# Performance work log

Measured on AMD Instinct MI355X. Metric: run time of the kernel, lower is better.

Reference implementation:

```python
import jax, jax.numpy as jnp
import numpy as np
from jax import lax

NW_LIST = [4, 8, 12]   # num_windows_list for num_windows=8
HEADS = 4
EPS = 1e-5             # BatchNorm eps (eval mode, running_mean=0, running_var=1)


def conv2d(x, w, pad):
    return lax.conv_general_dilated(x, w, (1, 1), [(pad, pad), (pad, pad)],
                                    dimension_numbers=('NCHW', 'OIHW', 'NCHW'))


def bn(x, g, b):
    # eval-mode BatchNorm with running_mean=0, running_var=1
    s = g / np.sqrt(1.0 + EPS)
    return x * s[None, :, None, None] + b[None, :, None, None]


def psa(x, q_w, k_w, v_w, proj_w):
    # multi-head spatial self-attention within a window, residual output
    B, C, h, w = x.shape
    L = h * w
    hd = C // HEADS
    q = conv2d(x, q_w, 0).reshape(B, HEADS, hd, L)
    k = conv2d(x, k_w, 0).reshape(B, HEADS, hd, L)
    v = conv2d(x, v_w, 0).reshape(B, HEADS, hd, L)
    attn = jax.nn.softmax(jnp.einsum('bhdl,bhdm->bhlm', q, k) * (hd ** -0.5), axis=-1)
    o = jnp.einsum('bhlm,bhdm->bhdl', attn, v).reshape(B, C, h, w)
    return conv2d(o, proj_w, 0) + x


def dpconv_forward(x, conv1_w, bn1_g, bn1_b, conv2_w, bn2_g, bn2_b,
                   conv3_w, bn3_g, bn3_b, pos_w, bnp_g, bnp_b,
                   q_w, k_w, v_w, proj_w):
    x1 = bn(conv2d(x, conv1_w, 0), bn1_g, bn1_b)
    chunks = jnp.split(x1, 3, axis=1)
    N, Cb, H, W = chunks[0].shape
    outs = []
    for nw, xc in zip(NW_LIST, chunks):
        sh, sw = H // nw, W // nw
        kh, kw = sh + H % nw, sw + W % nw
        hh = (np.arange(nw) * sh)[:, None] + np.arange(kh)   # [nw, kh] static indices
        ww = (np.arange(nw) * sw)[:, None] + np.arange(kw)   # [nw, kw]
        # unfold: [N,Cb,nw,kh,nw,kw] -> torch layout [N, Cb*kh*kw, L]
        p = xc[:, :, hh[:, :, None, None], ww[None, None, :, :]]
        u = p.transpose(0, 1, 3, 5, 2, 4).reshape(N, Cb * kh * kw, nw * nw)
        uw = u.reshape(-1, Cb, kh, kw)   # mirrors torch .view(-1, C, kh, kw)
        att = psa(uw, q_w, k_w, v_w, proj_w) + bn(conv2d(uw, pos_w, 1), bnp_g, bnp_b)
        y = att.reshape(N, Cb, kh, kw, nw, nw).transpose(0, 1, 4, 2, 5, 3)
        folded = jnp.zeros((N, Cb, H, W), x.dtype).at[
            :, :, hh[:, :, None, None], ww[None, None, :, :]].add(y)
        cnt = jnp.zeros((H, W), x.dtype).at[
            hh[:, :, None, None], ww[None, None, :, :]].add(
            jnp.ones((nw, kh, nw, kw), x.dtype))
        outs.append(folded / cnt[None, None])
    cat = jnp.concatenate(outs, axis=1)
    h2 = bn(conv2d(cat, conv2_w, 1), bn2_g, bn2_b) + x1
    return bn(conv2d(h2, conv3_w, 1), bn3_g, bn3_b)


def setup_inputs() -> dict:
    key = jax.random.key(0)
    ks = jax.random.split(key, 10)
    C, Cb = 192, 64
    inp = {
        'x': jax.random.normal(ks[0], (2, C, 100, 100), jnp.float32),
        'conv1_w': jax.random.normal(ks[1], (C, C, 1, 1), jnp.float32) * 0.05,
        'bn1_g': jnp.ones((C,), jnp.float32), 'bn1_b': jnp.zeros((C,), jnp.float32),
        'conv2_w': jax.random.normal(ks[2], (C, C, 3, 3), jnp.float32) * 0.05,
        'bn2_g': jnp.ones((C,), jnp.float32), 'bn2_b': jnp.zeros((C,), jnp.float32),
        'conv3_w': jax.random.normal(ks[3], (C, C, 3, 3), jnp.float32) * 0.05,
        'bn3_g': jnp.ones((C,), jnp.float32), 'bn3_b': jnp.zeros((C,), jnp.float32),
        'pos_w': jax.random.normal(ks[4], (Cb, Cb, 3, 3), jnp.float32) * 0.05,
        'bnp_g': jnp.ones((Cb,), jnp.float32), 'bnp_b': jnp.zeros((Cb,), jnp.float32),
        'q_w': jax.random.normal(ks[5], (Cb, Cb, 1, 1), jnp.float32) * 0.05,
        'k_w': jax.random.normal(ks[6], (Cb, Cb, 1, 1), jnp.float32) * 0.05,
        'v_w': jax.random.normal(ks[7], (Cb, Cb, 1, 1), jnp.float32) * 0.05,
        'proj_w': jax.random.normal(ks[8], (Cb, Cb, 1, 1), jnp.float32) * 0.05,
    }
    return inp


def reference(x, conv1_w, bn1_g, bn1_b, conv2_w, bn2_g, bn2_b,
              conv3_w, bn3_g, bn3_b, pos_w, bnp_g, bnp_b,
              q_w, k_w, v_w, proj_w):
    return dpconv_forward(x, conv1_w, bn1_g, bn1_b, conv2_w, bn2_g, bn2_b,
                          conv3_w, bn3_g, bn3_b, pos_w, bnp_g, bnp_b,
                          q_w, k_w, v_w, proj_w)
```

## Files before the change

### kernel.cpp

```cpp
#include <hip/hip_runtime.h>
#include <hip/hip_bf16.h>

#define N_ 2
#define C_ 192
#define CB_ 64
#define HW_ 100
#define PIX_ (HW_*HW_)
#define PADW_ 102
#define PADPIX_ (PADW_*PADW_)
#define KTOT_ 1728
#define KPOS_ 576
#define QSCALE_ 0.3606737602222409f

typedef __attribute__((ext_vector_type(8))) short bf16x8;
typedef __attribute__((ext_vector_type(4))) short bf16x4;
typedef __attribute__((ext_vector_type(4))) float f32x4;

#if defined(__has_builtin)
#if __has_builtin(__builtin_amdgcn_mfma_f32_16x16x16bf16_1k)
#define HAVE_MFMA16 1
#endif
#if __has_builtin(__builtin_amdgcn_exp2f)
#define EXP2(x) __builtin_amdgcn_exp2f(x)
#endif
#endif
#ifndef EXP2
#define EXP2(x) exp2f(x)
#endif

static __device__ __forceinline__ float bn_scale(float g) {
    return g * rsqrtf(1.0f + 1e-5f);
}

static __device__ __forceinline__ unsigned short f2bf(float v) {
    __hip_bfloat16 h = __float2bfloat16(v);
    return *(unsigned short*)&h;
}

__global__ __launch_bounds__(256) void x_nhwc_k(
    const float* __restrict__ in, unsigned short* __restrict__ out)
{
    int idx = blockIdx.x * 256 + threadIdx.x;
    if (idx >= N_ * 4 * PIX_) return;
    int p     = idx % PIX_;
    int chunk = (idx / PIX_) & 3;
    int n     = idx / (PIX_ * 4);
    int c0 = chunk * 48;
    const float* ip = in + ((size_t)n * C_ + c0) * PIX_ + p;
    unsigned short vals[48];
    #pragma unroll
    for (int j = 0; j < 48; ++j) vals[j] = f2bf(ip[(size_t)j * PIX_]);
    unsigned short* op = out + ((size_t)n * PIX_ + p) * 192 + c0;
    #pragma unroll
    for (int v = 0; v < 6; ++v) {
        bf16x8 pack;
        #pragma unroll
        for (int j = 0; j < 8; ++j) pack[j] = (short)vals[v * 8 + j];
        *(bf16x8*)(op + v * 8) = pack;
    }
}

__global__ __launch_bounds__(256) void conv1x1_mfma_k(
    const unsigned short* __restrict__ Xc,
    const float* __restrict__ w,
    const float* __restrict__ g, const float* __restrict__ bb,
    float* __restrict__ out)
{
    __shared__ unsigned short lds[64][72];
    int tid  = threadIdx.x;
    int lane = tid & 63;
    int wv   = tid >> 6;
    int c    = lane & 15;
    int g8   = (lane >> 4) * 8;
    int p0   = blockIdx.x * 64;
    int co0  = blockIdx.y * 64;
    int n    = blockIdx.z;

    int sp = tid >> 2;
    int sk = (tid & 3) * 8;
    int pc = min(p0 + sp, PIX_ - 1);
    const unsigned short* bp = Xc + ((size_t)n * PIX_ + pc) * 192;

    const float* arow = w + (size_t)(co0 + wv * 16 + c) * C_;

    f32x4 acc[4];
    #pragma unroll
    for (int f = 0; f < 4; ++f) acc[f] = (f32x4){0.f, 0.f, 0.f, 0.f};

    bf16x8 b0 = *(const bf16x8*)(bp + sk);
    bf16x8 b1 = *(const bf16x8*)(bp + 32 + sk);

    for (int k0 = 0; k0 < C_; k0 += 64) {
        __syncthreads();
        *(bf16x8*)(&lds[sp][sk])      = b0;
        *(bf16x8*)(&lds[sp][32 + sk]) = b1;
        __syncthreads();
        if (k0 + 64 < C_) {
            b0 = *(const bf16x8*)(bp + k0 + 64 + sk);
            b1 = *(const bf16x8*)(bp + k0 + 96 + sk);
        }
        #pragma unroll
        for (int h = 0; h < 2; ++h) {
            bf16x8 a;
            const float* ap = arow + k0 + h * 32 + g8;
            #pragma unroll
            for (int j = 0; j < 8; ++j) a[j] = (short)f2bf(ap[j]);
            #pragma unroll
            for (int f = 0; f < 4; ++f) {
                bf16x8 b = *(const bf16x8*)(&lds[f * 16 + c][h * 32 + g8]);
                acc[f] = __builtin_amdgcn_mfma_f32_16x16x32_bf16(a, b, acc[f], 0, 0, 0);
            }
        }
    }

    #pragma unroll
    for (int f = 0; f < 4; ++f) {
        int p = p0 + f * 16 + c;
        if (p < PIX_) {
            #pragma unroll
            for (int r = 0; r < 4; ++r) {
                int co = co0 + wv * 16 + (lane >> 4) * 4 + r;
                out[(size_t)(n * C_ + co) * PIX_ + p] = acc[f][r] * bn_scale(g[co]) + bb[co];
            }
        }
    }
}

__global__ __launch_bounds__(256) void wcvt_all_k(
    const float* __restrict__ pw, const float* __restrict__ w2,
    const float* __restrict__ w3,
    unsigned short* __restrict__ pwb, unsigned short* __restrict__ w2b,
    unsigned short* __restrict__ w3b)
{
    int idx = blockIdx.x * 256 + threadIdx.x;
    const int S0 = CB_ * KPOS_;
    const int S1 = S0 + C_ * KTOT_;
    const int S2 = S1 + C_ * KTOT_;
    if (idx < S0) {
        int t = idx % 9, ci = (idx / 9) % CB_, co = idx / (9 * CB_);
        pwb[(size_t)co * KPOS_ + t * CB_ + ci] = f2bf(pw[idx]);
    } else if (idx < S1) {
        int k = idx - S0;
        int t = k % 9, ci = (k / 9) % C_, co = k / (9 * C_);
        w2b[(size_t)co * KTOT_ + t * C_ + ci] = f2bf(w2[k]);
    } else if (idx < S2) {
        int k = idx - S1;
        int t = k % 9, ci = (k / 9) % C_, co = k / (9 * C_);
        w3b[(size_t)co * KTOT_ + t * C_ + ci] = f2bf(w3[k]);
    }
}

template<int NW, int SH, int KH>
__device__ __forceinline__ void gather_body(
    const float* __restrict__ x1, float* __restrict__ U, int f, int cidx)
{
    int t = f;
    int j = t % NW; t /= NW;
    int i = t % NW; t /= NW;
    int c = t % KH; t /= KH;
    int r = t % KH; t /= KH;
    int cb = t % CB_;
    int n  = t / CB_;
    int hh = i * SH + r;
    int ww = j * SH + c;
    U[f] = x1[((n * C_ + cidx * CB_ + cb) * HW_ + hh) * HW_ + ww];
}

__global__ __launch_bounds__(256) void gather_c_k(
    const float* __restrict__ x1, float* __restrict__ Uall)
{
    int gid = blockIdx.x * 256 + threadIdx.x;
    if (gid < 1280000)       gather_body<4, 25, 25>(x1, Uall,            gid,            0);
    else if (gid < 3377152)  gather_body<8, 12, 16>(x1, Uall + 1280000,  gid - 1280000,  1);
    else if (gid < 6031360)  gather_body<12, 8, 12>(x1, Uall + 3377152,  gid - 3377152,  2);
}

template<int L, int LP, int NPIX>
__device__ __forceinline__ void qkv_body(
    unsigned short (*lds)[72],
    const float* __restrict__ U,
    const float* __restrict__ qw, const float* __restrict__ kw,
    const float* __restrict__ vw,
    unsigned short* __restrict__ Q, unsigned short* __restrict__ Kt,
    unsigned short* __restrict__ V, int bid)
{
    int tid  = threadIdx.x;
    int lane = tid & 63;
    int wv   = tid >> 6;
    int c    = lane & 15;
    int g8   = (lane >> 4) * 8;
    int q0   = bid * 64;

    int sp = tid >> 2;
    int sk = (tid & 3) * 8;
    int qc = min(q0 + sp, NPIX - 1);
    int b  = qc / L, p = qc % L;
    const float* ub = U + (size_t)b * 64 * L + p;

    bf16x8 b0, b1;
    #pragma unroll
    for (int j = 0; j < 8; ++j) {
        b0[j] = (short)f2bf(ub[(size_t)(sk + j) * L]);
        b1[j] = (short)f2bf(ub[(size_t)(32 + sk + j) * L]);
    }
    __syncthreads();
    *(bf16x8*)(&lds[sp][sk])      = b0;
    *(bf16x8*)(&lds[sp][32 + sk]) = b1;
    __syncthreads();

    f32x4 acc[3][4];
    #pragma unroll
    for (int s = 0; s < 3; ++s)
        #pragma unroll
        for (int f = 0; f < 4; ++f) acc[s][f] = (f32x4){0.f, 0.f, 0.f, 0.f};

    const float* wbase[3] = {qw, kw, vw};
    #pragma unroll
    for (int s = 0; s < 3; ++s) {
        const float* arow = wbase[s] + (size_t)(wv * 16 + c) * 64;
        #pragma unroll
        for (int h = 0; h < 2; ++h) {
            bf16x8 a;
            const float* ap = arow + h * 32 + g8;
            #pragma unroll
            for (int j = 0; j < 8; ++j) a[j] = (short)f2bf(ap[j]);
            #pragma unroll
            for (int f = 0; f < 4; ++f) {
                bf16x8 bfr = *(const bf16x8*)(&lds[f * 16 + c][h * 32 + g8]);
                acc[s][f] = __builtin_amdgcn_mfma_f32_16x16x32_bf16(a, bfr, acc[s][f], 0, 0, 0);
            }
        }
    }

    #pragma unroll
    for (int f = 0; f < 4; ++f) {
        int qq = q0 + f * 16 + c;
        if (qq < NPIX) {
            int bo = qq / L, po = qq % L;
            #pragma unroll
            for (int r = 0; r < 4; ++r) {
                int co = wv * 16 + (lane >> 4) * 4 + r;
                Q[(size_t)(bo * 64 + co) * L + po] = f2bf(acc[0][f][r] * QSCALE_);
                Kt[((size_t)(bo * 4 + wv) * L + po) * 16 + ((lane >> 4) * 4 + r)] = f2bf(acc[1][f][r]);
                V[(size_t)(bo * 64 + co) * LP + po] = f2bf(acc[2][f][r]);
            }
        }
    }
}

__global__ __launch_bounds__(256) void qkv_c_k(
    const float* __restrict__ Uall,
    const float* __restrict__ qw, const float* __restrict__ kw,
    const float* __restrict__ vw,
    unsigned short* __restrict__ Qa, unsigned short* __restrict__ Ka,
    unsigned short* __restrict__ Va)
{
    __shared__ unsigned short lds[64][72];
    int bid = blockIdx.x;
    if (bid < 313)
        qkv_body<625, 632, 20000>(lds, Uall, qw, kw, vw, Qa, Ka, Va, bid);
    else if (bid < 825)
        qkv_body<256, 256, 32768>(lds, Uall + 1280000, qw, kw, vw,
                                  Qa + 1280000, Ka + 1280000, Va + 1294336, bid - 313);
    else
        qkv_body<144, 144, 41472>(lds, Uall + 3377152, qw, kw, vw,
                                  Qa + 3377152, Ka + 3377152, Va + 3391488, bid - 825);
}

template<int L, int LP, int NMT>
__device__ __forceinline__ void attn_body(
    const unsigned short* __restrict__ Q, const unsigned short* __restrict__ Kt,
    const unsigned short* __restrict__ V, unsigned short* __restrict__ O,
    int lblk, int bh)
{
    int tid  = threadIdx.x;
    int lane = tid & 63;
    int wv   = tid >> 6;
    int c    = lane & 15;
    int g    = lane >> 4;
    int b = bh >> 2, h = bh & 3;
    const unsigned short* qb = Q + (size_t)(b * 64 + h * 16) * L;
    const unsigned short* kb = Kt + (size_t)bh * L * 16;
    const unsigned short* vb = V + (size_t)(b * 64 + h * 16) * LP + (size_t)c * LP;
    unsigned short* ob = O + (size_t)(b * 64 + h * 16) * L;

    int l = lblk * 64 + wv * 16 + c;
    bool lval = (l < L);
    int lc = lval ? l : (L - 1);

    f32x4 acc = (f32x4){0.f, 0.f, 0.f, 0.f};
    float mrun = -1e30f, srun = 0.f;

#ifdef HAVE_MFMA16
    bf16x4 qf;
    #pragma unroll
    for (int j = 0; j < 4; ++j) qf[j] = (short)qb[(g * 4 + j) * L + lc];
#else
    bf16x8 qf = (bf16x8){0,0,0,0,0,0,0,0};
    if (g < 2) {
        #pragma unroll
        for (int j = 0; j < 8; ++j) qf[j] = (short)qb[(g * 8 + j) * L + lc];
    }
#endif

    for (int mt = 0; mt < NMT; ++mt) {
        int m0 = mt * 64;
        bool full = (m0 + 64 <= L);

        f32x4 s[4];
#ifdef HAVE_MFMA16
        #pragma unroll
        for (int t = 0; t < 4; ++t) {
            int mm = full ? (m0 + c + t * 16) : min(m0 + c + t * 16, L - 1);
            bf16x4 kf = *(const bf16x4*)(kb + (size_t)mm * 16 + g * 4);
            s[t] = __builtin_amdgcn_mfma_f32_16x16x16bf16_1k(
                kf, qf, (f32x4){0.f,0.f,0.f,0.f}, 0, 0, 0);
        }
#else
        #pragma unroll
        for (int t = 0; t < 4; ++t) {
            bf16x8 kf = (bf16x8){0,0,0,0,0,0,0,0};
            if (g < 2) {
                int mm = full ? (m0 + c + t * 16) : min(m0 + c + t * 16, L - 1);
                kf = *(const bf16x8*)(kb + (size_t)mm * 16 + g * 8);
            }
            s[t] = __builtin_amdgcn_mfma_f32_16x16x32_bf16(
                kf, qf, (f32x4){0.f,0.f,0.f,0.f}, 0, 0, 0);
        }
#endif

        float p[16];
        float tmax = -1e30f;
        #pragma unroll
        for (int t = 0; t < 4; ++t) {
            #pragma unroll
            for (int r = 0; r < 4; ++r) {
                int m = m0 + t * 16 + g * 4 + r;
                float v = s[t][r];
                if (!full && m >= L) v = -1e30f;
                p[t * 4 + r] = v;
                tmax = fmaxf(tmax, v);
            }
        }
        tmax = fmaxf(tmax, __shfl_xor(tmax, 16, 64));
        tmax = fmaxf(tmax, __shfl_xor(tmax, 32, 64));
        if (!__all(tmax <= mrun)) {
            float mnew = fmaxf(mrun, tmax);
            float corr = EXP2(mrun - mnew);
            srun *= corr;
            #pragma unroll
            for (int r = 0; r < 4; ++r) acc[r] *= corr;
            mrun = mnew;
        }
        float ps0 = 0.f, ps1 = 0.f, ps2 = 0.f, ps3 = 0.f;
        #pragma unroll
        for (int t = 0; t < 4; ++t) {
            p[t * 4 + 0] = EXP2(p[t * 4 + 0] - mrun); ps0 += p[t * 4 + 0];
            p[t * 4 + 1] = EXP2(p[t * 4 + 1] - mrun); ps1 += p[t * 4 + 1];
            p[t * 4 + 2] = EXP2(p[t * 4 + 2] - mrun); ps2 += p[t * 4 + 2];
            p[t * 4 + 3] = EXP2(p[t * 4 + 3] - mrun); ps3 += p[t * 4 + 3];
        }
        srun += (ps0 + ps1) + (ps2 + ps3);

#ifdef HAVE_MFMA16
        #pragma unroll
        for (int t = 0; t < 4; ++t) {
            bf16x4 pb;
            #pragma unroll
            for (int j = 0; j < 4; ++j) pb[j] = (short)f2bf(p[t * 4 + j]);
            bf16x4 vf = *(const bf16x4*)(vb + m0 + t * 16 + g * 4);
            acc = __builtin_amdgcn_mfma_f32_16x16x16bf16_1k(vf, pb, acc, 0, 0, 0);
        }
#else
        int hi = g >> 1;
        #pragma unroll
        for (int H = 0; H < 2; ++H) {
            bf16x8 pb;
            #pragma unroll
            for (int j = 0; j < 8; ++j) {
                int srcLane = (((2 * g + (j >> 2)) & 3) << 4) | c;
                float v1 = __shfl(p[(H * 2) * 4 + (j & 3)], srcLane, 64);
                float v2 = __shfl(p[(H * 2 + 1) * 4 + (j & 3)], srcLane, 64);
                pb[j] = (short)f2bf(hi ? v2 : v1);
            }
            bf16x8 vf = *(const bf16x8*)(vb + m0 + H * 32 + g * 8);
            acc = __builtin_amdgcn_mfma_f32_16x16x32_bf16(vf, pb, acc, 0, 0, 0);
        }
#endif
    }

    float stot = srun;
    stot += __shfl_xor(stot, 16, 64);
    stot += __shfl_xor(stot, 32, 64);
    float inv = 1.f / stot;
    if (lval) {
        #pragma unroll
        for (int r = 0; r < 4; ++r)
            ob[(size_t)(g * 4 + r) * L + l] = f2bf(acc[r] * inv);
    }
}

__global__ __launch_bounds__(256) void attn_c_k(
    const unsigned short* __restrict__ Qa, const unsigned short* __restrict__ Ka,
    const unsigned short* __restrict__ Va, unsigned short* __restrict__ Oa)
{
    int bid = blockIdx.x;
    if (bid < 1280) {
        attn_body<625, 632, 10>(Qa, Ka, Va, Oa, bid % 10, bid / 10);
    } else if (bid < 3328) {
        int k = bid - 1280;
        attn_body<256, 256, 4>(Qa + 1280000, Ka + 1280000, Va + 1294336,
                               Oa + 1280000, k % 4, k / 4);
    } else {
        int k = bid - 3328;
        attn_body<144, 144, 3>(Qa + 3377152, Ka + 3377152, Va + 3391488,
                               Oa + 3377152, k % 3, k / 3);
    }
}

template<int L, int NPIX>
__device__ __forceinline__ void proj_body(
    unsigned short (*lds)[72],
    const unsigned short* __restrict__ O, const float* __restrict__ U,
    const float* __restrict__ pw, float* __restrict__ A, int bid)
{
    int tid  = threadIdx.x;
    int lane = tid & 63;
    int wv   = tid >> 6;
    int c    = lane & 15;
    int g8   = (lane >> 4) * 8;
    int q0   = bid * 64;

    int sp = tid >> 2;
    int sk = (tid & 3) * 8;
    int qc = min(q0 + sp, NPIX - 1);
    int b  = qc / L, p = qc % L;
    const unsigned short* ob = O + (size_t)b * 64 * L + p;

    bf16x8 b0, b1;
    #pragma unroll
    for (int j = 0; j < 8; ++j) {
        b0[j] = (short)ob[(size_t)(sk + j) * L];
        b1[j] = (short)ob[(size_t)(32 + sk + j) * L];
    }
    __syncthreads();
    *(bf16x8*)(&lds[sp][sk])      = b0;
    *(bf16x8*)(&lds[sp][32 + sk]) = b1;
    __syncthreads();

    f32x4 acc[4];
    #pragma unroll
    for (int f = 0; f < 4; ++f) acc[f] = (f32x4){0.f, 0.f, 0.f, 0.f};

    const float* arow = pw + (size_t)(wv * 16 + c) * 64;
    #pragma unroll
    for (int h = 0; h < 2; ++h) {
        bf16x8 a;
        const float* ap = arow + h * 32 + g8;
        #pragma unroll
        for (int j = 0; j < 8; ++j) a[j] = (short)f2bf(ap[j]);
        #pragma unroll
        for (int f = 0; f < 4; ++f) {
            bf16x8 bfr = *(const bf16x8*)(&lds[f * 16 + c][h * 32 + g8]);
            acc[f] = __builtin_amdgcn_mfma_f32_16x16x32_bf16(a, bfr, acc[f], 0, 0, 0);
        }
    }

    #pragma unroll
    for (int f = 0; f < 4; ++f) {
        int qq = q0 + f * 16 + c;
        if (qq < NPIX) {
            int bo = qq / L, po = qq % L;
            #pragma unroll
            for (int r = 0; r < 4; ++r) {
                int co = wv * 16 + (lane >> 4) * 4 + r;
                size_t oi = (size_t)(bo * 64 + co) * L + po;
                A[oi] = acc[f][r] + U[oi];
            }
        }
    }
}

__global__ __launch_bounds__(256) void proj_c_k(
    const unsigned short* __restrict__ Oa, const float* __restrict__ Uall,
    const float* __restrict__ pw, float* __restrict__ Aa)
{
    __shared__ unsigned short lds[64][72];
    int bid = blockIdx.x;
    if (bid < 313)
        proj_body<625, 20000>(lds, Oa, Uall, pw, Aa, bid);
    else if (bid < 825)
        proj_body<256, 32768>(lds, Oa + 1280000, Uall + 1280000, pw, Aa + 1280000, bid - 313);
    else
        proj_body<144, 41472>(lds, Oa + 3377152, Uall + 3377152, pw, Aa + 3377152, bid - 825);
}

template<int KH, int PW, int L>
__device__ __forceinline__ void padU_body(
    const float* __restrict__ U, unsigned short* __restrict__ Up, int idx)
{
    int pp = idx % (PW * PW);
    int b  = idx / (PW * PW);
    int xx = pp % PW, yy = pp / PW;
    bool inter = (xx >= 1 && xx <= KH && yy >= 1 && yy <= KH);
    const float* up = U + (size_t)b * 64 * L + (yy - 1) * KH + (xx - 1);
    unsigned short vals[64];
    #pragma unroll
    for (int j = 0; j < 64; ++j) vals[j] = inter ? f2bf(up[(size_t)j * L]) : 0;
    unsigned short* op = Up + (size_t)idx * 64;
    #pragma unroll
    for (int v = 0; v < 8; ++v) {
        bf16x8 pack;
        #pragma unroll
        for (int j = 0; j < 8; ++j) pack[j] = (short)vals[v * 8 + j];
        *(bf16x8*)(op + v * 8) = pack;
    }
}

__global__ __launch_bounds__(256) void padU_c_k(
    const float* __restrict__ Uall, unsigned short* __restrict__ Upa)
{
    int idx = blockIdx.x * 256 + threadIdx.x;
    if (idx < 23328)        padU_body<25, 27, 625>(Uall,            Upa,            idx);
    else if (idx < 64800)   padU_body<16, 18, 256>(Uall + 1280000,  Upa + 1492992,  idx - 23328);
    else if (idx < 121248)  padU_body<12, 14, 144>(Uall + 3377152,  Upa + 4147200,  idx - 64800);
}

template<int L, int PW, int KH, int NPIX>
__device__ __forceinline__ void posconv_body(
    unsigned short (*lds)[64][72],
    const unsigned short* __restrict__ Up, const unsigned short* __restrict__ Wb,
    const float* __restrict__ g, const float* __restrict__ bb,
    float* __restrict__ A, int bid)
{
    int tid  = threadIdx.x;
    int lane = tid & 63;
    int wv   = tid >> 6;
    int c    = lane & 15;
    int g8   = (lane >> 4) * 8;
    int p0   = bid * 64;

    int sp = tid >> 2;
    int sk = (tid & 3) * 8;
    int qq0 = p0 + sp;
    int po = 0;
    if (qq0 < NPIX) {
        int b = qq0 / L, p = qq0 % L;
        po = b * PW * PW + (p / KH) * PW + (p % KH);
    }

    const unsigned short* arow = Wb + (size_t)(wv * 16 + c) * KPOS_;

    f32x4 acc[4];
    #pragma unroll
    for (int f = 0; f < 4; ++f) acc[f] = (f32x4){0.f, 0.f, 0.f, 0.f};

    const int NT = KPOS_ / 64;

    bf16x8 b0, b1, a0, a1;
    {
        const unsigned short* bp = Up + ((size_t)po << 6);
        b0 = *(const bf16x8*)(bp + sk);
        b1 = *(const bf16x8*)(bp + 32 + sk);
        *(bf16x8*)(&lds[0][sp][sk])      = b0;
        *(bf16x8*)(&lds[0][sp][32 + sk]) = b1;
    }
    {
        const unsigned short* bp = Up + ((size_t)(po + 1) << 6);
        b0 = *(const bf16x8*)(bp + sk);
        b1 = *(const bf16x8*)(bp + 32 + sk);
    }
    a0 = *(const bf16x8*)(arow + g8);
    a1 = *(const bf16x8*)(arow + 32 + g8);

    for (int t = 0; t < NT; ++t) {
        __syncthreads();
        bf16x8 bf0[4], bf1[4];
        #pragma unroll
        for (int f = 0; f < 4; ++f) {
            bf0[f] = *(const bf16x8*)(&lds[t & 1][f * 16 + c][g8]);
            bf1[f] = *(const bf16x8*)(&lds[t & 1][f * 16 + c][32 + g8]);
        }
        if (t + 1 < NT) {
            *(bf16x8*)(&lds[(t + 1) & 1][sp][sk])      = b0;
            *(bf16x8*)(&lds[(t + 1) & 1][sp][32 + sk]) = b1;
            if (t + 2 < NT) {
                int tap = t + 2;
                int toff = (tap / 3) * PW + (tap % 3);
                const unsigned short* bp = Up + ((size_t)(po + toff) << 6);
                b0 = *(const bf16x8*)(bp + sk);
                b1 = *(const bf16x8*)(bp + 32 + sk);
            }
        }
        bf16x8 a0n, a1n;
        if (t + 1 < NT) {
            a0n = *(const bf16x8*)(arow + (t + 1) * 64 + g8);
            a1n = *(const bf16x8*)(arow + (t + 1) * 64 + 32 + g8);
        }
        #pragma unroll
        for (int f = 0; f < 4; ++f) {
            acc[f] = __builtin_amdgcn_mfma_f32_16x16x32_bf16(a0, bf0[f], acc[f], 0, 0, 0);
            acc[f] = __builtin_amdgcn_mfma_f32_16x16x32_bf16(a1, bf1[f], acc[f], 0, 0, 0);
        }
        a0 = a0n; a1 = a1n;
    }

    #pragma unroll
    for (int f = 0; f < 4; ++f) {
        int q = p0 + f * 16 + c;
        if (q < NPIX) {
            int b = q / L, p = q % L;
            #pragma unroll
            for (int r = 0; r < 4; ++r) {
                int co = wv * 16 + (lane >> 4) * 4 + r;
                A[(size_t)(b * 64 + co) * L + p] += acc[f][r] * bn_scale(g[co]) + bb[co];
            }
        }
    }
}

__global__ __launch_bounds__(256) void posconv_c_k(
    const unsigned short* __restrict__ Upa, const unsigned short* __restrict__ Wb,
    const float* __restrict__ g, const float* __restrict__ bb,
    float* __restrict__ Aa)
{
    __shared__ unsigned short lds[2][64][72];
    int bid = blockIdx.x;
    if (bid < 313)
        posconv_body<625, 27, 25, 20000>(lds, Upa, Wb, g, bb, Aa, bid);
    else if (bid < 825)
        posconv_body<256, 18, 16, 32768>(lds, Upa + 1492992, Wb, g, bb, Aa + 1280000, bid - 313);
    else
        posconv_body<144, 14, 12, 41472>(lds, Upa + 4147200, Wb, g, bb, Aa + 3377152, bid - 825);
}

template<int NW, int SH, int KH>
__device__ __forceinline__ void fold_body(
    const float* __restrict__ A, float* __restrict__ cat, int idx, int cidx)
{
    int w  = idx % HW_;
    int h  = (idx / HW_) % HW_;
    int cb = (idx / PIX_) % CB_;
    int n  = idx / (PIX_ * CB_);
    int numh = h - KH + 1;
    int ilo = numh > 0 ? (numh + SH - 1) / SH : 0;
    int ihi = min(NW - 1, h / SH);
    int numw = w - KH + 1;
    int jlo = numw > 0 ? (numw + SH - 1) / SH : 0;
    int jhi = min(NW - 1, w / SH);
    float sum = 0.f;
    for (int i = ilo; i <= ihi; ++i) {
        int r = h - i * SH;
        for (int j = jlo; j <= jhi; ++j) {
            int c = w - j * SH;
            int f = ((((n * CB_ + cb) * KH + r) * KH + c) * NW + i) * NW + j;
            sum += A[f];
        }
    }
    float cnt = (float)((ihi - ilo + 1) * (jhi - jlo + 1));
    cat[((n * C_ + cidx * CB_ + cb) * HW_ + h) * HW_ + w] = sum / cnt;
}

__global__ __launch_bounds__(256) void fold_c_k(
    const float* __restrict__ Aa, float* __restrict__ cat)
{
    int idx = blockIdx.x * 256 + threadIdx.x;
    if (idx < 1280000)       fold_body<4, 25, 25>(Aa,            cat, idx,            0);
    else if (idx < 2560000)  fold_body<8, 12, 16>(Aa + 1280000,  cat, idx - 1280000,  1);
    else if (idx < 3840000)  fold_body<12, 8, 12>(Aa + 3377152,  cat, idx - 2560000,  2);
}

__global__ __launch_bounds__(256) void pad_nhwc_k(
    const float* __restrict__ in, unsigned short* __restrict__ out)
{
    int idx = blockIdx.x * 256 + threadIdx.x;
    if (idx >= N_ * 4 * PADPIX_) return;
    int pp    = idx % PADPIX_;
    int chunk = (idx / PADPIX_) & 3;
    int n     = idx / (PADPIX_ * 4);
    int xx = pp % PADW_, yy = pp / PADW_;
    int c0 = chunk * 48;
    bool inter = (xx >= 1 && xx <= HW_ && yy >= 1 && yy <= HW_);
    const float* ip = in + ((size_t)n * C_ + c0) * PIX_ + (yy - 1) * HW_ + (xx - 1);
    unsigned short vals[48];
    #pragma unroll
    for (int j = 0; j < 48; ++j) vals[j] = inter ? f2bf(ip[(size_t)j * PIX_]) : 0;
    unsigned short* op = out + ((size_t)n * PADPIX_ + pp) * 192 + c0;
    #pragma unroll
    for (int v = 0; v < 6; ++v) {
        bf16x8 pack;
        #pragma unroll
        for (int j = 0; j < 8; ++j) pack[j] = (short)vals[v * 8 + j];
        *(bf16x8*)(op + v * 8) = pack;
    }
}

__global__ __launch_bounds__(256) void ring_zero_k(unsigned short* __restrict__ Xb)
{
    int idx = blockIdx.x * 256 + threadIdx.x;
    if (idx >= N_ * 404 * 192) return;
    int cc = idx % 192;
    int rp = (idx / 192) % 404;
    int n  = idx / (192 * 404);
    int yy, xx;
    if (rp < 102)      { yy = 0;            xx = rp; }
    else if (rp < 204) { yy = 101;          xx = rp - 102; }
    else if (rp < 304) { yy = rp - 204 + 1; xx = 0; }
    else               { yy = rp - 304 + 1; xx = 101; }
    Xb[((size_t)n * PADPIX_ + yy * PADW_ + xx) * 192 + cc] = 0;
}

#define NB3_ (157*3*2)
template<bool RES, bool TOXB>
__global__ __launch_bounds__(256) void conv3x3_mfma_k(
    const unsigned short* __restrict__ Xp,
    const unsigned short* __restrict__ Wb,
    const float* __restrict__ g, const float* __restrict__ bb,
    const float* __restrict__ res, float* __restrict__ out,
    unsigned short* __restrict__ xout)
{
    __shared__ unsigned short lds[2][64][72];
    int tid  = threadIdx.x;
    int lane = tid & 63;
    int wv   = tid >> 6;
    int c    = lane & 15;
    int g8   = (lane >> 4) * 8;

    const int q = NB3_ / 8, r = NB3_ % 8;
    int gid  = blockIdx.x;
    int xcd  = gid % 8, slot = gid / 8;
    int wgid = (xcd < r) ? xcd * (q + 1) + slot
                         : r * (q + 1) + (xcd - r) * q + slot;
    int co0  = (wgid % 3) * 64;
    int rest = wgid / 3;
    int p0   = (rest % 157) * 64;
    int n    = rest / 157;

    const unsigned short* Xn = Xp + (size_t)n * PADPIX_ * 192;

    int sp = tid >> 2;
    int sk = (tid & 3) * 8;
    int pix = p0 + sp;
    int po = (pix < PIX_) ? (pix / HW_) * PADW_ + (pix % HW_) : 0;

    const unsigned short* arow = Wb + (size_t)(co0 + wv * 16 + c) * KTOT_;

    f32x4 acc[4];
    #pragma unroll
    for (int f = 0; f < 4; ++f) acc[f] = (f32x4){0.f, 0.f, 0.f, 0.f};

    const int NT = KTOT_ / 64;

    bf16x8 b0, b1, a0, a1;
    {
        const unsigned short* bp = Xn + (size_t)po * 192;
        b0 = *(const bf16x8*)(bp + sk);
        b1 = *(const bf16x8*)(bp + 32 + sk);
        *(bf16x8*)(&lds[0][sp][sk])      = b0;
        *(bf16x8*)(&lds[0][sp][32 + sk]) = b1;
    }
    {
        const unsigned short* bp = Xn + (size_t)po * 192 + 64;
        b0 = *(const bf16x8*)(bp + sk);
        b1 = *(const bf16x8*)(bp + 32 + sk);
    }
    a0 = *(const bf16x8*)(arow + g8);
    a1 = *(const bf16x8*)(arow + 32 + g8);

    for (int t = 0; t < NT; ++t) {
        __syncthreads();
        bf16x8 bf0[4], bf1[4];
        #pragma unroll
        for (int f = 0; f < 4; ++f) {
            bf0[f] = *(const bf16x8*)(&lds[t & 1][f * 16 + c][g8]);
            bf1[f] = *(const bf16x8*)(&lds[t & 1][f * 16 + c][32 + g8]);
        }
        if (t + 1 < NT) {
            *(bf16x8*)(&lds[(t + 1) & 1][sp][sk])      = b0;
            *(bf16x8*)(&lds[(t + 1) & 1][sp][32 + sk]) = b1;
            if (t + 2 < NT) {
                int k2 = (t + 2) * 64;
                int tap = k2 / 192;
                int ci0 = k2 - tap * 192;
                int toff = (tap / 3) * PADW_ + (tap % 3);
                const unsigned short* bp = Xn + (size_t)(po + toff) * 192 + ci0;
                b0 = *(const bf16x8*)(bp + sk);
                b1 = *(const bf16x8*)(bp + 32 + sk);
            }
        }
        bf16x8 a0n, a1n;
        if (t + 1 < NT) {
            a0n = *(const bf16x8*)(arow + (t + 1) * 64 + g8);
            a1n = *(const bf16x8*)(arow + (t + 1) * 64 + 32 + g8);
        }
        #pragma unroll
        for (int f = 0; f < 4; ++f) {
            acc[f] = __builtin_amdgcn_mfma_f32_16x16x32_bf16(a0, bf0[f], acc[f], 0, 0, 0);
            acc[f] = __builtin_amdgcn_mfma_f32_16x16x32_bf16(a1, bf1[f], acc[f], 0, 0, 0);
        }
        a0 = a0n; a1 = a1n;
    }

    #pragma unroll
    for (int f = 0; f < 4; ++f) {
        int p = p0 + f * 16 + c;
        if (p < PIX_) {
            if (TOXB) {
                int py = p / HW_, px = p % HW_;
                unsigned short* o = xout +
                    ((size_t)n * PADPIX_ + (py + 1) * PADW_ + (px + 1)) * 192 +
                    co0 + wv * 16 + (lane >> 4) * 4;
                ushort4 pk;
                #pragma unroll
                for (int r2 = 0; r2 < 4; ++r2) {
                    int co = co0 + wv * 16 + (lane >> 4) * 4 + r2;
                    float v = acc[f][r2] * bn_scale(g[co]) + bb[co];
                    if (RES) v += res[(size_t)(n * C_ + co) * PIX_ + p];
                    ((unsigned short*)&pk)[r2] = f2bf(v);
                }
                *(ushort4*)o = pk;
            } else {
                #pragma unroll
                for (int r2 = 0; r2 < 4; ++r2) {
                    int co = co0 + wv * 16 + (lane >> 4) * 4 + r2;
                    float v = acc[f][r2] * bn_scale(g[co]) + bb[co];
                    if (RES) v += res[(size_t)(n * C_ + co) * PIX_ + p];
                    out[(size_t)(n * C_ + co) * PIX_ + p] = v;
                }
            }
        }
    }
}

extern "C" void kernel_launch(void* const* d_in, const int* in_sizes, int n_in,
                              void* d_out, int out_size, void* d_ws, size_t ws_size,
                              hipStream_t stream) {
    const float* x       = (const float*)d_in[0];
    const float* conv1_w = (const float*)d_in[1];
    const float* bn1_g   = (const float*)d_in[2];
    const float* bn1_b   = (const float*)d_in[3];
    const float* conv2_w = (const float*)d_in[4];
    const float* bn2_g   = (const float*)d_in[5];
    const float* bn2_b   = (const float*)d_in[6];
    const float* conv3_w = (const float*)d_in[7];
    const float* bn3_g   = (const float*)d_in[8];
    const float* bn3_b   = (const float*)d_in[9];
    const float* pos_w   = (const float*)d_in[10];
    const float* bnp_g   = (const float*)d_in[11];
    const float* bnp_b   = (const float*)d_in[12];
    const float* q_w     = (const float*)d_in[13];
    const float* k_w     = (const float*)d_in[14];
    const float* v_w     = (const float*)d_in[15];
    const float* proj_w  = (const float*)d_in[16];

    float* ws = (float*)d_ws;
    float* x1   = ws;
    float* cat  = ws + 3840000;
    unsigned short* Xc    = (unsigned short*)(ws + 7680000);
    float* Uall = ws + 9600000;
    unsigned short* Oall  = (unsigned short*)(ws + 15640000);
    float* Aall = ws + 21680000;
    unsigned short* Qall  = (unsigned short*)(ws + 27720000);
    unsigned short* Ktall = (unsigned short*)(ws + 30740000);
    unsigned short* Vall  = (unsigned short*)(ws + 33760000);
    unsigned short* Upall = (unsigned short*)(ws + 36790000);
    unsigned short* pwb   = (unsigned short*)(ws + 40670000);
    unsigned short* w2b   = (unsigned short*)(ws + 40690000);
    unsigned short* w3b   = (unsigned short*)(ws + 40856000);
    unsigned short* Xb    = (unsigned short*)(ws + 41022000);
    unsigned short* Xb2   = (unsigned short*)(ws + 43020000);

    x_nhwc_k<<<(N_ * 4 * PIX_ + 255) / 256, 256, 0, stream>>>(x, Xc);
    conv1x1_mfma_k<<<dim3(157, 3, 2), 256, 0, stream>>>(Xc, conv1_w, bn1_g, bn1_b, x1);
    wcvt_all_k<<<(700416 + 255) / 256, 256, 0, stream>>>(pos_w, conv2_w, conv3_w, pwb, w2b, w3b);

    gather_c_k<<<(6031360 + 255) / 256, 256, 0, stream>>>(x1, Uall);
    qkv_c_k<<<1473, 256, 0, stream>>>(Uall, q_w, k_w, v_w, Qall, Ktall, Vall);
    attn_c_k<<<6784, 256, 0, stream>>>(Qall, Ktall, Vall, Oall);
    proj_c_k<<<1473, 256, 0, stream>>>(Oall, Uall, proj_w, Aall);
    padU_c_k<<<(121248 + 255) / 256, 256, 0, stream>>>(Uall, Upall);
    posconv_c_k<<<1473, 256, 0, stream>>>(Upall, pwb, bnp_g, bnp_b, Aall);
    fold_c_k<<<(3840000 + 255) / 256, 256, 0, stream>>>(Aall, cat);

    pad_nhwc_k<<<(N_ * 4 * PADPIX_ + 255) / 256, 256, 0, stream>>>(cat, Xb);
    ring_zero_k<<<(N_ * 404 * 192 + 255) / 256, 256, 0, stream>>>(Xb2);
    conv3x3_mfma_k<true, true><<<NB3_, 256, 0, stream>>>(
        Xb, w2b, bn2_g, bn2_b, x1, nullptr, Xb2);
    conv3x3_mfma_k<false, false><<<NB3_, 256, 0, stream>>>(
        Xb2, w3b, bn3_g, bn3_b, nullptr, (float*)d_out, nullptr);
}
```

Before: 305.2 us.

## Process two query tiles per wave in attention to reuse K/V loads

Each wave in the windowed attention kernel now handles two 16-query chunks, 64 rows apart, so every block covers 128 query positions instead of 64. Each K and V fragment loaded from global memory feeds two MFMA chains, and the online-softmax state is kept per chunk. The grid shrinks to match the new coverage. The cost is higher register pressure, and more wasted work in the smallest window group, where 144 queries are padded to 256.

```diff
diff --git a/kernel.cpp b/kernel.cpp
--- a/kernel.cpp
+++ b/kernel.cpp
@@ -284,22 +284,39 @@
     const unsigned short* vb = V + (size_t)(b * 64 + h * 16) * LP + (size_t)c * LP;
     unsigned short* ob = O + (size_t)(b * 64 + h * 16) * L;
 
-    int l = lblk * 64 + wv * 16 + c;
-    bool lval = (l < L);
-    int lc = lval ? l : (L - 1);
-
-    f32x4 acc = (f32x4){0.f, 0.f, 0.f, 0.f};
-    float mrun = -1e30f, srun = 0.f;
+    int lbase = lblk * 128 + wv * 16 + c;
+    int l[2] = {lbase, lbase + 64};
+    bool lval[2];
+    int lc[2];
+    #pragma unroll
+    for (int ch = 0; ch < 2; ++ch) {
+        lval[ch] = (l[ch] < L);
+        lc[ch] = lval[ch] ? l[ch] : (L - 1);
+    }
+
+    f32x4 acc[2];
+    float mrun[2], srun[2];
+    #pragma unroll
+    for (int ch = 0; ch < 2; ++ch) {
+        acc[ch] = (f32x4){0.f, 0.f, 0.f, 0.f};
+        mrun[ch] = -1e30f; srun[ch] = 0.f;
+    }
 
 #ifdef HAVE_MFMA16
-    bf16x4 qf;
-    #pragma unroll
-    for (int j = 0; j < 4; ++j) qf[j] = (short)qb[(g * 4 + j) * L + lc];
+    bf16x4 qf[2];
+    #pragma unroll
+    for (int ch = 0; ch < 2; ++ch)
+        #pragma unroll
+        for (int j = 0; j < 4; ++j) qf[ch][j] = (short)qb[(g * 4 + j) * L + lc[ch]];
 #else
-    bf16x8 qf = (bf16x8){0,0,0,0,0,0,0,0};
-    if (g < 2) {
-        #pragma unroll
-        for (int j = 0; j < 8; ++j) qf[j] = (short)qb[(g * 8 + j) * L + lc];
+    bf16x8 qf[2];
+    #pragma unroll
+    for (int ch = 0; ch < 2; ++ch) {
+        qf[ch] = (bf16x8){0,0,0,0,0,0,0,0};
+        if (g < 2) {
+            #pragma unroll
+            for (int j = 0; j < 8; ++j) qf[ch][j] = (short)qb[(g * 8 + j) * L + lc[ch]];
+        }
     }
 #endif
 
@@ -307,14 +324,21 @@
         int m0 = mt * 64;
         bool full = (m0 + 64 <= L);
 
-        f32x4 s[4];
+        float p[2][16];
 #ifdef HAVE_MFMA16
         #pragma unroll
         for (int t = 0; t < 4; ++t) {
             int mm = full ? (m0 + c + t * 16) : min(m0 + c + t * 16, L - 1);
             bf16x4 kf = *(const bf16x4*)(kb + (size_t)mm * 16 + g * 4);
-            s[t] = __builtin_amdgcn_mfma_f32_16x16x16bf16_1k(
-                kf, qf, (f32x4){0.f,0.f,0.f,0.f}, 0, 0, 0);
+            f32x4 s0 = __builtin_amdgcn_mfma_f32_16x16x16bf16_1k(
+                kf, qf[0], (f32x4){0.f,0.f,0.f,0.f}, 0, 0, 0);
+            f32x4 s1 = __builtin_amdgcn_mfma_f32_16x16x16bf16_1k(
+                kf, qf[1], (f32x4){0.f,0.f,0.f,0.f}, 0, 0, 0);
+            #pragma unroll
+            for (int r = 0; r < 4; ++r) {
+                p[0][t * 4 + r] = s0[r];
+                p[1][t * 4 + r] = s1[r];
+            }
         }
 #else
         #pragma unroll
@@ -324,79 +348,98 @@
                 int mm = full ? (m0 + c + t * 16) : min(m0 + c + t * 16, L - 1);
                 kf = *(const bf16x8*)(kb + (size_t)mm * 16 + g * 8);
             }
-            s[t] = __builtin_amdgcn_mfma_f32_16x16x32_bf16(
-                kf, qf, (f32x4){0.f,0.f,0.f,0.f}, 0, 0, 0);
+            f32x4 s0 = __builtin_amdgcn_mfma_f32_16x16x32_bf16(
+                kf, qf[0], (f32x4){0.f,0.f,0.f,0.f}, 0, 0, 0);
+            f32x4 s1 = __builtin_amdgcn_mfma_f32_16x16x32_bf16(
+                kf, qf[1], (f32x4){0.f,0.f,0.f,0.f}, 0, 0, 0);
+            #pragma unroll
+            for (int r = 0; r < 4; ++r) {
+                p[0][t * 4 + r] = s0[r];
+                p[1][t * 4 + r] = s1[r];
+            }
         }
 #endif
 
-        float p[16];
-        float tmax = -1e30f;
+        #pragma unroll
+        for (int ch = 0; ch < 2; ++ch) {
+            float tmax = -1e30f;
+            #pragma unroll
+            for (int t = 0; t < 4; ++t) {
+                #pragma unroll
+                for (int r = 0; r < 4; ++r) {
+                    int m = m0 + t * 16 + g * 4 + r;
+                    float v = p[ch][t * 4 + r];
+                    if (!full && m >= L) v = -1e30f;
+                    p[ch][t * 4 + r] = v;
+                    tmax = fmaxf(tmax, v);
+                }
+            }
+            tmax = fmaxf(tmax, __shfl_xor(tmax, 16, 64));
+            tmax = fmaxf(tmax, __shfl_xor(tmax, 32, 64));
+            if (!__all(tmax <= mrun[ch])) {
+                float mnew = fmaxf(mrun[ch], tmax);
+                float corr = EXP2(mrun[ch] - mnew);
+                srun[ch] *= corr;
+                #pragma unroll
+                for (int r = 0; r < 4; ++r) acc[ch][r] *= corr;
+                mrun[ch] = mnew;
+            }
+            float ps0 = 0.f, ps1 = 0.f, ps2 = 0.f, ps3 = 0.f;
+            #pragma unroll
+            for (int t = 0; t < 4; ++t) {
+                p[ch][t * 4 + 0] = EXP2(p[ch][t * 4 + 0] - mrun[ch]); ps0 += p[ch][t * 4 + 0];
+                p[ch][t * 4 + 1] = EXP2(p[ch][t * 4 + 1] - mrun[ch]); ps1 += p[ch][t * 4 + 1];
+                p[ch][t * 4 + 2] = EXP2(p[ch][t * 4 + 2] - mrun[ch]); ps2 += p[ch][t * 4 + 2];
+                p[ch][t * 4 + 3] = EXP2(p[ch][t * 4 + 3] - mrun[ch]); ps3 += p[ch][t * 4 + 3];
+            }
+            srun[ch] += (ps0 + ps1) + (ps2 + ps3);
+        }
+
+#ifdef HAVE_MFMA16
         #pragma unroll
         for (int t = 0; t < 4; ++t) {
-            #pragma unroll
-            for (int r = 0; r < 4; ++r) {
-                int m = m0 + t * 16 + g * 4 + r;
-                float v = s[t][r];
-                if (!full && m >= L) v = -1e30f;
-                p[t * 4 + r] = v;
-                tmax = fmaxf(tmax, v);
-            }
-        }
-        tmax = fmaxf(tmax, __shfl_xor(tmax, 16, 64));
-        tmax = fmaxf(tmax, __shfl_xor(tmax, 32, 64));
-        if (!__all(tmax <= mrun)) {
-            float mnew = fmaxf(mrun, tmax);
-            float corr = EXP2(mrun - mnew);
-            srun *= corr;
-            #pragma unroll
-            for (int r = 0; r < 4; ++r) acc[r] *= corr;
-            mrun = mnew;
-        }
-        float ps0 = 0.f, ps1 = 0.f, ps2 = 0.f, ps3 = 0.f;
-        #pragma unroll
-        for (int t = 0; t < 4; ++t) {
-            p[t * 4 + 0] = EXP2(p[t * 4 + 0] - mrun); ps0 += p[t * 4 + 0];
-            p[t * 4 + 1] = EXP2(p[t * 4 + 1] - mrun); ps1 += p[t * 4 + 1];
-            p[t * 4 + 2] = EXP2(p[t * 4 + 2] - mrun); ps2 += p[t * 4 + 2];
-            p[t * 4 + 3] = EXP2(p[t * 4 + 3] - mrun); ps3 += p[t * 4 + 3];
-        }
-        srun += (ps0 + ps1) + (ps2 + ps3);
-
-#ifdef HAVE_MFMA16
-        #pragma unroll
-        for (int t = 0; t < 4; ++t) {
-            bf16x4 pb;
-            #pragma unroll
-            for (int j = 0; j < 4; ++j) pb[j] = (short)f2bf(p[t * 4 + j]);
             bf16x4 vf = *(const bf16x4*)(vb + m0 + t * 16 + g * 4);
-            acc = __builtin_amdgcn_mfma_f32_16x16x16bf16_1k(vf, pb, acc, 0, 0, 0);
+            bf16x4 pb0, pb1;
+            #pragma unroll
+            for (int j = 0; j < 4; ++j) {
+                pb0[j] = (short)f2bf(p[0][t * 4 + j]);
+                pb1[j] = (short)f2bf(p[1][t * 4 + j]);
+            }
+            acc[0] = __builtin_amdgcn_mfma_f32_16x16x16bf16_1k(vf, pb0, acc[0], 0, 0, 0);
+            acc[1] = __builtin_amdgcn_mfma_f32_16x16x16bf16_1k(vf, pb1, acc[1], 0, 0, 0);
         }
 #else
         int hi = g >> 1;
         #pragma unroll
         for (int H = 0; H < 2; ++H) {
-            bf16x8 pb;
-            #pragma unroll
-            for (int j = 0; j < 8; ++j) {
-                int srcLane = (((2 * g + (j >> 2)) & 3) << 4) | c;
-                float v1 = __shfl(p[(H * 2) * 4 + (j & 3)], srcLane, 64);
-                float v2 = __shfl(p[(H * 2 + 1) * 4 + (j & 3)], srcLane, 64);
-                pb[j] = (short)f2bf(hi ? v2 : v1);
-            }
             bf16x8 vf = *(const bf16x8*)(vb + m0 + H * 32 + g * 8);
-            acc = __builtin_amdgcn_mfma_f32_16x16x32_bf16(vf, pb, acc, 0, 0, 0);
+            #pragma unroll
+            for (int ch = 0; ch < 2; ++ch) {
+                bf16x8 pb;
+                #pragma unroll
+                for (int j = 0; j < 8; ++j) {
+                    int srcLane = (((2 * g + (j >> 2)) & 3) << 4) | c;
+                    float v1 = __shfl(p[ch][(H * 2) * 4 + (j & 3)], srcLane, 64);
+                    float v2 = __shfl(p[ch][(H * 2 + 1) * 4 + (j & 3)], srcLane, 64);
+                    pb[j] = (short)f2bf(hi ? v2 : v1);
+                }
+                acc[ch] = __builtin_amdgcn_mfma_f32_16x16x32_bf16(vf, pb, acc[ch], 0, 0, 0);
+            }
         }
 #endif
     }
 
-    float stot = srun;
-    stot += __shfl_xor(stot, 16, 64);
-    stot += __shfl_xor(stot, 32, 64);
-    float inv = 1.f / stot;
-    if (lval) {
-        #pragma unroll
-        for (int r = 0; r < 4; ++r)
-            ob[(size_t)(g * 4 + r) * L + l] = f2bf(acc[r] * inv);
+    #pragma unroll
+    for (int ch = 0; ch < 2; ++ch) {
+        float stot = srun[ch];
+        stot += __shfl_xor(stot, 16, 64);
+        stot += __shfl_xor(stot, 32, 64);
+        float inv = 1.f / stot;
+        if (lval[ch]) {
+            #pragma unroll
+            for (int r = 0; r < 4; ++r)
+                ob[(size_t)(g * 4 + r) * L + l[ch]] = f2bf(acc[ch][r] * inv);
+        }
     }
 }
 
@@ -405,16 +448,16 @@
     const unsigned short* __restrict__ Va, unsigned short* __restrict__ Oa)
 {
     int bid = blockIdx.x;
-    if (bid < 1280) {
-        attn_body<625, 632, 10>(Qa, Ka, Va, Oa, bid % 10, bid / 10);
-    } else if (bid < 3328) {
-        int k = bid - 1280;
+    if (bid < 640) {
+        attn_body<625, 632, 10>(Qa, Ka, Va, Oa, bid % 5, bid / 5);
+    } else if (bid < 1664) {
+        int k = bid - 640;
         attn_body<256, 256, 4>(Qa + 1280000, Ka + 1280000, Va + 1294336,
-                               Oa + 1280000, k % 4, k / 4);
+                               Oa + 1280000, k % 2, k / 2);
     } else {
-        int k = bid - 3328;
+        int k = bid - 1664;
         attn_body<144, 144, 3>(Qa + 3377152, Ka + 3377152, Va + 3391488,
-                               Oa + 3377152, k % 3, k / 3);
+                               Oa + 3377152, k % 2, k / 2);
     }
 }
 
@@ -876,7 +919,7 @@
 
     gather_c_k<<<(6031360 + 255) / 256, 256, 0, stream>>>(x1, Uall);
     qkv_c_k<<<1473, 256, 0, stream>>>(Uall, q_w, k_w, v_w, Qall, Ktall, Vall);
-    attn_c_k<<<6784, 256, 0, stream>>>(Qall, Ktall, Vall, Oall);
+    attn_c_k<<<2688 + 1280, 256, 0, stream>>>(Qall, Ktall, Vall, Oall);
     proj_c_k<<<1473, 256, 0, stream>>>(Oall, Uall, proj_w, Aall);
     padU_c_k<<<(121248 + 255) / 256, 256, 0, stream>>>(Uall, Upall);
     posconv_c_k<<<1473, 256, 0, stream>>>(Upall, pwb, bnp_g, bnp_b, Aall);
```

Measured after the change: 293.7 us. -3.8%, faster.
